# Optimization experiments

Hardware: AMD Instinct MI355X
Metric: run time of the kernel (lower is better)

The kernel has to match this reference:

```python
import jax, jax.numpy as jnp
import numpy as np

K = 1024
EPS = 1e-6


def _offdiag_idx(k):
    # row-major (i outer, j inner) indices with i != j, matching the torch double loop order
    idx = np.arange(k * k)
    return jnp.asarray(idx[(idx // k) != (idx % k)])


def pair_features(boxes):
    # boxes: [K, 4] = (x, y, w, h). Returns [K*(K-1), 13] pairwise features.
    x, y, w, h = boxes[:, 0], boxes[:, 1], boxes[:, 2], boxes[:, 3]
    xi, yi, wi, hi = x[:, None], y[:, None], w[:, None], h[:, None]  # i index -> rows
    xj, yj, wj, hj = x[None, :], y[None, :], w[None, :], h[None, :]  # j index -> cols

    dx = (xj - xi) / wi
    dy = (yj - yi) / hi
    dw = jnp.log(wj / wi + EPS)
    dh = jnp.log(hj / hi + EPS)

    x2i, y2i = xi + wi, yi + hi
    x2j, y2j = xj + wj, yj + hj
    inter_w = jnp.maximum(0.0, jnp.minimum(x2i, x2j) - jnp.maximum(xi, xj))
    inter_h = jnp.maximum(0.0, jnp.minimum(y2i, y2j) - jnp.maximum(yi, yj))
    inter = inter_w * inter_h
    union = wi * hi + wj * hj - inter
    iou = inter / (union + EPS)

    ones = jnp.ones_like(dx)
    feats = jnp.stack(
        [dx, dy, dw, dh,
         wi * ones, hi * ones, wj * ones, hj * ones,
         iou,
         xi * ones, yi * ones, xj * ones, yj * ones],
        axis=-1,
    )  # [K, K, 13]
    k = boxes.shape[0]
    return feats.reshape(k * k, 13)[_offdiag_idx(k)]  # [K*(K-1), 13]


def setup_inputs() -> dict:
    key = jax.random.key(0)
    kb, k1, k2, k3, k4 = jax.random.split(key, 5)
    xy = jax.random.uniform(kb, (K, 2), dtype=jnp.float32) * 100.0
    wh = jax.random.uniform(jax.random.fold_in(kb, 1), (K, 2), dtype=jnp.float32) * 50.0 + 1.0
    boxes = jnp.concatenate([xy, wh], axis=1)  # [K, 4], positive w/h
    in_dim, out_dim = 13, 128
    W1 = jax.random.normal(k1, (in_dim, out_dim), dtype=jnp.float32) / np.sqrt(in_dim)
    b1 = jax.random.normal(k2, (out_dim,), dtype=jnp.float32) * 0.01
    W2 = jax.random.normal(k3, (out_dim, out_dim), dtype=jnp.float32) / np.sqrt(out_dim)
    b2 = jax.random.normal(k4, (out_dim,), dtype=jnp.float32) * 0.01
    return {"boxes": boxes, "W1": W1, "b1": b1, "W2": W2, "b2": b2}


def reference(boxes, W1, b1, W2, b2):
    feats = pair_features(boxes)                       # [K*(K-1), 13]
    h = jax.nn.relu(feats @ W1 + b1)                   # [K*(K-1), 128]
    return h @ W2 + b2                                 # [K*(K-1), 128]
```

## Files before the change

kernel.cpp:

```cpp
#include <hip/hip_runtime.h>
#include <hip/hip_bf16.h>

#define KBOX 1024
#define KM1  1023
#define NROWS (KBOX * KM1)
#define BM   32
#define HD   128
#define LDH  136
#define THREADS 256
#define NBLOCK (NROWS / BM)

typedef __attribute__((ext_vector_type(8))) short bf16x8;
typedef __attribute__((ext_vector_type(4))) float floatx4;

__global__ void prep_w2(const float* __restrict__ W2, __hip_bfloat16* __restrict__ w2t) {
    int idx = blockIdx.x * blockDim.x + threadIdx.x;
    int n = idx >> 7;
    int k = idx & 127;
    w2t[n * HD + k] = __float2bfloat16(W2[k * HD + n]);
}

__global__ __launch_bounds__(THREADS, 3)
void pair_mlp(const float* __restrict__ boxes,
              const float* __restrict__ W1,
              const float* __restrict__ b1,
              const __hip_bfloat16* __restrict__ w2t,
              const float* __restrict__ b2,
              float* __restrict__ out) {
    __shared__ __align__(16) __hip_bfloat16 sW2[HD * LDH];
    __shared__ __align__(16) __hip_bfloat16 sHhi[BM * LDH];
    __shared__ __align__(16) __hip_bfloat16 sHlo[BM * LDH];
    __shared__ __align__(16) float sFeat[BM * 16];

    const int tid = threadIdx.x;
    const int p0  = blockIdx.x * BM;

    #pragma unroll
    for (int it = 0; it < 8; ++it) {
        int c  = tid + it * THREADS;
        int n  = c >> 4;
        int kc = c & 15;
        bf16x8 v = *(const bf16x8*)(w2t + n * HD + kc * 8);
        *(bf16x8*)(&sW2[n * LDH + kc * 8]) = v;
    }

    if (tid < BM) {
        unsigned r   = (unsigned)(p0 + tid);
        unsigned i   = r / KM1;
        unsigned rem = r - i * KM1;
        unsigned j   = rem + (rem >= i ? 1u : 0u);
        float4 bi = *(const float4*)(boxes + 4u * i);
        float4 bj = *(const float4*)(boxes + 4u * j);
        float xi = bi.x, yi = bi.y, wi = bi.z, hi = bi.w;
        float xj = bj.x, yj = bj.y, wj = bj.z, hj = bj.w;
        float dx = (xj - xi) / wi;
        float dy = (yj - yi) / hi;
        float dw = logf(wj / wi + 1e-6f);
        float dh = logf(hj / hi + 1e-6f);
        float iw = fmaxf(0.0f, fminf(xi + wi, xj + wj) - fmaxf(xi, xj));
        float ih = fmaxf(0.0f, fminf(yi + hi, yj + hj) - fmaxf(yi, yj));
        float inter = iw * ih;
        float uni   = wi * hi + wj * hj - inter;
        float iou   = inter / (uni + 1e-6f);
        float f[13] = {dx, dy, dw, dh, wi, hi, wj, hj, iou, xi, yi, xj, yj};
        #pragma unroll
        for (int t = 0; t < 13; ++t) sFeat[tid * 16 + t] = f[t];
    }

    const int c     = tid & 127;
    const int phalf = tid >> 7;
    float w1c[13];
    #pragma unroll
    for (int f = 0; f < 13; ++f) w1c[f] = W1[f * HD + c];
    const float b1c = b1[c];

    __syncthreads();

    #pragma unroll
    for (int pi = 0; pi < 16; ++pi) {
        int p = phalf + pi * 2;
        const float4* fp = (const float4*)(&sFeat[p * 16]);
        float4 f0 = fp[0], f1 = fp[1], f2 = fp[2];
        float f12 = sFeat[p * 16 + 12];
        float ff[13] = {f0.x, f0.y, f0.z, f0.w, f1.x, f1.y, f1.z, f1.w,
                        f2.x, f2.y, f2.z, f2.w, f12};
        float h = b1c;
        #pragma unroll
        for (int f = 0; f < 13; ++f) h = fmaf(ff[f], w1c[f], h);
        h = fmaxf(h, 0.0f);
        __hip_bfloat16 hh = __float2bfloat16(h);
        float hr = h - __bfloat162float(hh);
        __hip_bfloat16 hl = __float2bfloat16(hr);
        sHhi[p * LDH + c] = hh;
        sHlo[p * LDH + c] = hl;
    }

    __syncthreads();

    const int lane  = tid & 63;
    const int wave  = tid >> 6;
    const int waveM = wave & 1;
    const int waveN = wave >> 1;
    const int lr    = lane & 15;
    const int quad  = lane >> 4;

    floatx4 acc[4] = {{0.f,0.f,0.f,0.f},{0.f,0.f,0.f,0.f},
                      {0.f,0.f,0.f,0.f},{0.f,0.f,0.f,0.f}};

    const int arow = waveM * 16 + lr;
    #pragma unroll
    for (int ks = 0; ks < 4; ++ks) {
        int kb = ks * 32 + quad * 8;
        bf16x8 ahi = *(const bf16x8*)(&sHhi[arow * LDH + kb]);
        bf16x8 alo = *(const bf16x8*)(&sHlo[arow * LDH + kb]);
        #pragma unroll
        for (int nt = 0; nt < 4; ++nt) {
            int ncol = waveN * 64 + nt * 16 + lr;
            bf16x8 b = *(const bf16x8*)(&sW2[ncol * LDH + kb]);
            acc[nt] = __builtin_amdgcn_mfma_f32_16x16x32_bf16(ahi, b, acc[nt], 0, 0, 0);
            acc[nt] = __builtin_amdgcn_mfma_f32_16x16x32_bf16(alo, b, acc[nt], 0, 0, 0);
        }
    }

    #pragma unroll
    for (int nt = 0; nt < 4; ++nt) {
        int ncol   = waveN * 64 + nt * 16 + lr;
        float bias = b2[ncol];
        #pragma unroll
        for (int reg = 0; reg < 4; ++reg) {
            int prow = waveM * 16 + quad * 4 + reg;
            out[(size_t)(p0 + prow) * HD + ncol] = acc[nt][reg] + bias;
        }
    }
}

extern "C" void kernel_launch(void* const* d_in, const int* in_sizes, int n_in,
                              void* d_out, int out_size, void* d_ws, size_t ws_size,
                              hipStream_t stream) {
    (void)in_sizes; (void)n_in; (void)out_size; (void)ws_size;
    const float* boxes = (const float*)d_in[0];
    const float* W1    = (const float*)d_in[1];
    const float* b1    = (const float*)d_in[2];
    const float* W2    = (const float*)d_in[3];
    const float* b2    = (const float*)d_in[4];
    float* out = (float*)d_out;
    __hip_bfloat16* w2t = (__hip_bfloat16*)d_ws;

    prep_w2<<<64, 256, 0, stream>>>(W2, w2t);
    pair_mlp<<<NBLOCK, THREADS, 0, stream>>>(boxes, W1, b1, w2t, b2, out);
}
```

Before: 663.4 us.

## Rewrite pair MLP as persistent multi-tile kernel with MFMA first layer

Each block now processes 8 tiles of 32 pair rows instead of one. Every thread computes features for its own row, and the first layer runs as split-bf16 MFMAs using W1 halves precomputed by the prep kernel. W2 is read directly from global or L2 instead of being staged into shared memory per block. Hidden activations go to a swizzled, double-buffered shared buffer, and the output uses vectorized float4 stores in a transposed tile orientation. This removes the per-block W2 staging, the scalar FMA first layer and the scalar output stores, at the cost of repeated global W2 loads and reduced-precision __logf.

New measurement: 771.8 us. 16.4% more time.

```diff
diff --git a/kernel.cpp b/kernel.cpp
--- a/kernel.cpp
+++ b/kernel.cpp
@@ -1,136 +1,158 @@
 #include <hip/hip_runtime.h>
 #include <hip/hip_bf16.h>
 
-#define KBOX 1024
-#define KM1  1023
-#define NROWS (KBOX * KM1)
-#define BM   32
-#define HD   128
-#define LDH  136
+#define KM1   1023
+#define NROWS (1024 * 1023)
+#define TILE  32
+#define TPB   8
 #define THREADS 256
-#define NBLOCK (NROWS / BM)
+#define NBLOCK (NROWS / (TILE * TPB))
 
 typedef __attribute__((ext_vector_type(8))) short bf16x8;
 typedef __attribute__((ext_vector_type(4))) float floatx4;
 
-__global__ void prep_w2(const float* __restrict__ W2, __hip_bfloat16* __restrict__ w2t) {
-    int idx = blockIdx.x * blockDim.x + threadIdx.x;
-    int n = idx >> 7;
-    int k = idx & 127;
-    w2t[n * HD + k] = __float2bfloat16(W2[k * HD + n]);
+__device__ __forceinline__ unsigned short f2bf(float f) {
+    return __builtin_bit_cast(unsigned short, __float2bfloat16(f));
+}
+__device__ __forceinline__ float bf2f(unsigned short u) {
+    return __builtin_bit_cast(float, (unsigned)u << 16);
 }
 
-__global__ __launch_bounds__(THREADS, 3)
+__global__ void prep(const float* __restrict__ W1, const float* __restrict__ W2,
+                     unsigned short* __restrict__ ws) {
+    int idx = blockIdx.x * 256 + threadIdx.x;
+    if (idx < 16384) {
+        int n = idx >> 7, k = idx & 127;
+        ws[n * 128 + k] = f2bf(W2[k * 128 + n]);
+    } else {
+        int j = idx - 16384;
+        int c = j >> 5, k = j & 31;
+        float v = (k < 13) ? W1[k * 128 + c] : 0.0f;
+        unsigned short hi = f2bf(v);
+        ws[16384 + c * 32 + k] = hi;
+        ws[20480 + c * 32 + k] = f2bf(v - bf2f(hi));
+    }
+}
+
+__global__ __launch_bounds__(THREADS, 4)
 void pair_mlp(const float* __restrict__ boxes,
-              const float* __restrict__ W1,
               const float* __restrict__ b1,
-              const __hip_bfloat16* __restrict__ w2t,
               const float* __restrict__ b2,
+              const unsigned short* __restrict__ wsro,
               float* __restrict__ out) {
-    __shared__ __align__(16) __hip_bfloat16 sW2[HD * LDH];
-    __shared__ __align__(16) __hip_bfloat16 sHhi[BM * LDH];
-    __shared__ __align__(16) __hip_bfloat16 sHlo[BM * LDH];
-    __shared__ __align__(16) float sFeat[BM * 16];
+    __shared__ __align__(16) unsigned short sH[2][2][32 * 128];
 
-    const int tid = threadIdx.x;
-    const int p0  = blockIdx.x * BM;
+    const unsigned short* w2t   = wsro;
+    const unsigned short* w1thi = wsro + 16384;
+    const unsigned short* w1tlo = wsro + 20480;
 
-    #pragma unroll
-    for (int it = 0; it < 8; ++it) {
-        int c  = tid + it * THREADS;
-        int n  = c >> 4;
-        int kc = c & 15;
-        bf16x8 v = *(const bf16x8*)(w2t + n * HD + kc * 8);
-        *(bf16x8*)(&sW2[n * LDH + kc * 8]) = v;
-    }
+    const int tid   = threadIdx.x;
+    const int lane  = tid & 63;
+    const int wave  = tid >> 6;
+    const int phalf = wave & 1;
+    const int nh    = wave >> 1;
+    const int lr    = lane & 15;
+    const int q     = lane >> 4;
+    const int p     = phalf * 16 + lr;
+    const int swz   = lr << 4;
+    const int rowb  = p << 8;
+    const unsigned pbase = blockIdx.x * (TILE * TPB);
 
-    if (tid < BM) {
-        unsigned r   = (unsigned)(p0 + tid);
-        unsigned i   = r / KM1;
-        unsigned rem = r - i * KM1;
-        unsigned j   = rem + (rem >= i ? 1u : 0u);
-        float4 bi = *(const float4*)(boxes + 4u * i);
-        float4 bj = *(const float4*)(boxes + 4u * j);
-        float xi = bi.x, yi = bi.y, wi = bi.z, hi = bi.w;
-        float xj = bj.x, yj = bj.y, wj = bj.z, hj = bj.w;
+    for (int t = 0; t < TPB; ++t) {
+        char* hbase = (char*)&sH[t & 1][0][0];
+        char* lbase = hbase + 8192;
+
+        const unsigned r = pbase + t * TILE + p;
+        unsigned bi_ = r / KM1;
+        unsigned rem = r - bi_ * KM1;
+        unsigned bj_ = rem + (rem >= bi_ ? 1u : 0u);
+        float4 bA = *(const float4*)(boxes + 4u * bi_);
+        float4 bB = *(const float4*)(boxes + 4u * bj_);
+        float xi = bA.x, yi = bA.y, wi = bA.z, hi = bA.w;
+        float xj = bB.x, yj = bB.y, wj = bB.z, hj = bB.w;
         float dx = (xj - xi) / wi;
         float dy = (yj - yi) / hi;
-        float dw = logf(wj / wi + 1e-6f);
-        float dh = logf(hj / hi + 1e-6f);
+        float dw = __logf(wj / wi + 1e-6f);
+        float dh = __logf(hj / hi + 1e-6f);
         float iw = fmaxf(0.0f, fminf(xi + wi, xj + wj) - fmaxf(xi, xj));
         float ih = fmaxf(0.0f, fminf(yi + hi, yj + hj) - fmaxf(yi, yj));
         float inter = iw * ih;
         float uni   = wi * hi + wj * hj - inter;
         float iou   = inter / (uni + 1e-6f);
-        float f[13] = {dx, dy, dw, dh, wi, hi, wj, hj, iou, xi, yi, xj, yj};
+
+        float fA[8] = {dx, dy, dw, dh, wi, hi, wj, hj};
+        float fB[8] = {iou, xi, yi, xj, yj, 0.f, 0.f, 0.f};
+        bf16x8 Fhi, Flo;
         #pragma unroll
-        for (int t = 0; t < 13; ++t) sFeat[tid * 16 + t] = f[t];
-    }
+        for (int e = 0; e < 8; ++e) {
+            float v = (q == 0) ? fA[e] : ((q == 1) ? fB[e] : 0.0f);
+            unsigned short vh = f2bf(v);
+            Fhi[e] = (short)vh;
+            Flo[e] = (short)f2bf(v - bf2f(vh));
+        }
 
-    const int c     = tid & 127;
-    const int phalf = tid >> 7;
-    float w1c[13];
-    #pragma unroll
-    for (int f = 0; f < 13; ++f) w1c[f] = W1[f * HD + c];
-    const float b1c = b1[c];
+        {
+            bf16x8 whi[4], wlo[4];
+            floatx4 a1[4];
+            #pragma unroll
+            for (int m = 0; m < 4; ++m) {
+                const int mt = nh * 4 + m;
+                const int c  = mt * 16 + lr;
+                whi[m] = *(const bf16x8*)(w1thi + c * 32 + q * 8);
+                wlo[m] = *(const bf16x8*)(w1tlo + c * 32 + q * 8);
+                a1[m]  = *(const floatx4*)(b1 + mt * 16 + q * 4);
+            }
+            #pragma unroll
+            for (int m = 0; m < 4; ++m) {
+                a1[m] = __builtin_amdgcn_mfma_f32_16x16x32_bf16(whi[m], Fhi, a1[m], 0, 0, 0);
+                a1[m] = __builtin_amdgcn_mfma_f32_16x16x32_bf16(whi[m], Flo, a1[m], 0, 0, 0);
+                a1[m] = __builtin_amdgcn_mfma_f32_16x16x32_bf16(wlo[m], Fhi, a1[m], 0, 0, 0);
+            }
+            #pragma unroll
+            for (int m = 0; m < 4; ++m) {
+                const int mt = nh * 4 + m;
+                unsigned short hh[4], hl[4];
+                #pragma unroll
+                for (int e = 0; e < 4; ++e) {
+                    float h = fmaxf(a1[m][e], 0.0f);
+                    hh[e] = f2bf(h);
+                    hl[e] = f2bf(h - bf2f(hh[e]));
+                }
+                const int kb = (mt * 32 + q * 8) ^ swz;
+                uint2 uh, ul;
+                uh.x = (unsigned)hh[0] | ((unsigned)hh[1] << 16);
+                uh.y = (unsigned)hh[2] | ((unsigned)hh[3] << 16);
+                ul.x = (unsigned)hl[0] | ((unsigned)hl[1] << 16);
+                ul.y = (unsigned)hl[2] | ((unsigned)hl[3] << 16);
+                *(uint2*)(hbase + rowb + kb) = uh;
+                *(uint2*)(lbase + rowb + kb) = ul;
+            }
+        }
 
-    __syncthreads();
+        __syncthreads();
 
-    #pragma unroll
-    for (int pi = 0; pi < 16; ++pi) {
-        int p = phalf + pi * 2;
-        const float4* fp = (const float4*)(&sFeat[p * 16]);
-        float4 f0 = fp[0], f1 = fp[1], f2 = fp[2];
-        float f12 = sFeat[p * 16 + 12];
-        float ff[13] = {f0.x, f0.y, f0.z, f0.w, f1.x, f1.y, f1.z, f1.w,
-                        f2.x, f2.y, f2.z, f2.w, f12};
-        float h = b1c;
+        floatx4 a2[4];
         #pragma unroll
-        for (int f = 0; f < 13; ++f) h = fmaf(ff[f], w1c[f], h);
-        h = fmaxf(h, 0.0f);
-        __hip_bfloat16 hh = __float2bfloat16(h);
-        float hr = h - __bfloat162float(hh);
-        __hip_bfloat16 hl = __float2bfloat16(hr);
-        sHhi[p * LDH + c] = hh;
-        sHlo[p * LDH + c] = hl;
-    }
+        for (int nt = 0; nt < 4; ++nt)
+            a2[nt] = *(const floatx4*)(b2 + nh * 64 + nt * 16 + q * 4);
+        #pragma unroll
+        for (int ks = 0; ks < 4; ++ks) {
+            const int kb = (ks * 64 + q * 16) ^ swz;
+            bf16x8 Bhi = *(const bf16x8*)(hbase + rowb + kb);
+            bf16x8 Blo = *(const bf16x8*)(lbase + rowb + kb);
+            #pragma unroll
+            for (int nt = 0; nt < 4; ++nt) {
+                const int n = nh * 64 + nt * 16 + lr;
+                bf16x8 A2 = *(const bf16x8*)(w2t + n * 128 + ks * 32 + q * 8);
+                a2[nt] = __builtin_amdgcn_mfma_f32_16x16x32_bf16(A2, Bhi, a2[nt], 0, 0, 0);
+                a2[nt] = __builtin_amdgcn_mfma_f32_16x16x32_bf16(A2, Blo, a2[nt], 0, 0, 0);
+            }
+        }
 
-    __syncthreads();
-
-    const int lane  = tid & 63;
-    const int wave  = tid >> 6;
-    const int waveM = wave & 1;
-    const int waveN = wave >> 1;
-    const int lr    = lane & 15;
-    const int quad  = lane >> 4;
-
-    floatx4 acc[4] = {{0.f,0.f,0.f,0.f},{0.f,0.f,0.f,0.f},
-                      {0.f,0.f,0.f,0.f},{0.f,0.f,0.f,0.f}};
-
-    const int arow = waveM * 16 + lr;
-    #pragma unroll
-    for (int ks = 0; ks < 4; ++ks) {
-        int kb = ks * 32 + quad * 8;
-        bf16x8 ahi = *(const bf16x8*)(&sHhi[arow * LDH + kb]);
-        bf16x8 alo = *(const bf16x8*)(&sHlo[arow * LDH + kb]);
+        float* orow = out + (size_t)(pbase + t * TILE + p) * 128 + nh * 64 + q * 4;
         #pragma unroll
-        for (int nt = 0; nt < 4; ++nt) {
-            int ncol = waveN * 64 + nt * 16 + lr;
-            bf16x8 b = *(const bf16x8*)(&sW2[ncol * LDH + kb]);
-            acc[nt] = __builtin_amdgcn_mfma_f32_16x16x32_bf16(ahi, b, acc[nt], 0, 0, 0);
-            acc[nt] = __builtin_amdgcn_mfma_f32_16x16x32_bf16(alo, b, acc[nt], 0, 0, 0);
-        }
-    }
-
-    #pragma unroll
-    for (int nt = 0; nt < 4; ++nt) {
-        int ncol   = waveN * 64 + nt * 16 + lr;
-        float bias = b2[ncol];
-        #pragma unroll
-        for (int reg = 0; reg < 4; ++reg) {
-            int prow = waveM * 16 + quad * 4 + reg;
-            out[(size_t)(p0 + prow) * HD + ncol] = acc[nt][reg] + bias;
-        }
+        for (int nt = 0; nt < 4; ++nt)
+            *(floatx4*)(orow + nt * 16) = a2[nt];
     }
 }
 
@@ -144,8 +166,8 @@
     const float* W2    = (const float*)d_in[3];
     const float* b2    = (const float*)d_in[4];
     float* out = (float*)d_out;
-    __hip_bfloat16* w2t = (__hip_bfloat16*)d_ws;
+    unsigned short* ws = (unsigned short*)d_ws;
 
-    prep_w2<<<64, 256, 0, stream>>>(W2, w2t);
-    pair_mlp<<<NBLOCK, THREADS, 0, stream>>>(boxes, W1, b1, w2t, b2, out);
+    prep<<<80, THREADS, 0, stream>>>(W1, W2, ws);
+    pair_mlp<<<NBLOCK, THREADS, 0, stream>>>(boxes, b1, b2, ws, out);
 }
```
